# Kernel optimization log

Hardware: AMD Instinct MI355X
Metric: run time of the kernel (lower is better)

The kernel has to match this reference:

```python
import jax, jax.numpy as jnp
import numpy as np

N = 100000      # nodes per type
E = 1600000     # edges per edge type
D = 128         # input feature dim
C = 128         # hidden channels (heads=1, concat)
DE = 16         # edge feature dim
OUT = 64        # out channels
L = 2           # num conv layers
T = 2           # num edge types: 0 = user->item, 1 = item->user


def setup_inputs() -> dict:
    key = jax.random.key(0)
    ks = jax.random.split(key, 17)
    s = 0.05  # keep attention logits / activations well-scaled
    return {
        "x_user": jax.random.normal(ks[0], (N, D), jnp.float32),
        "x_item": jax.random.normal(ks[1], (N, D), jnp.float32),
        "ea_ui": jax.random.normal(ks[2], (E, DE), jnp.float32),
        "ea_iu": jax.random.normal(ks[3], (E, DE), jnp.float32),
        "W_src": jax.random.normal(ks[4], (L, T, C, C), jnp.float32) * s,
        "W_dst": jax.random.normal(ks[5], (L, T, C, C), jnp.float32) * s,
        "W_edge": jax.random.normal(ks[6], (L, T, DE, C), jnp.float32) * s,
        "att_src": jax.random.normal(ks[7], (L, T, C), jnp.float32) * s,
        "att_dst": jax.random.normal(ks[8], (L, T, C), jnp.float32) * s,
        "att_edge": jax.random.normal(ks[9], (L, T, C), jnp.float32) * s,
        "conv_bias": jax.random.normal(ks[10], (L, T, C), jnp.float32) * s,
        "lin0_W": jax.random.normal(ks[11], (2, C, C), jnp.float32) * s,
        "lin0_b": jax.random.normal(ks[12], (2, C), jnp.float32) * s,
        "lin1_W": jax.random.normal(ks[13], (2, C, OUT), jnp.float32) * s,
        "lin1_b": jax.random.normal(ks[14], (2, OUT), jnp.float32) * s,
        "ei_ui": jax.random.randint(ks[15], (2, E), 0, N, jnp.int32),
        "ei_iu": jax.random.randint(ks[16], (2, E), 0, N, jnp.int32),
    }


def _gat_conv(x_src, x_dst, ei, ea, Ws, Wd, We, a_s, a_d, a_e, b):
    """PyG GATConv((-1,-1), C, heads=1, edge_dim=DE, add_self_loops=False)."""
    row, col = ei[0], ei[1]
    hs = x_src @ Ws                      # [Ns, C]
    hd = x_dst @ Wd                      # [Nd, C]
    he = ea @ We                         # [E, C]
    a = hs @ a_s                         # [Ns] alpha_src per source node
    adst = hd @ a_d                      # [Nd] alpha_dst per dest node
    ae = he @ a_e                        # [E]
    alpha = jax.nn.leaky_relu(a[row] + adst[col] + ae, 0.2)  # [E]
    n_dst = x_dst.shape[0]
    m = jax.ops.segment_max(alpha, col, num_segments=n_dst)  # stable softmax max
    ex = jnp.exp(alpha - m[col])
    den = jax.ops.segment_sum(ex, col, num_segments=n_dst)
    w = ex / den[col]                    # edge-softmax over incoming edges
    out = jax.ops.segment_sum(w[:, None] * hs[row], col, num_segments=n_dst)
    return out + b                       # [Nd, C]


def reference(x_user, x_item, ea_ui, ea_iu, W_src, W_dst, W_edge, att_src,
              att_dst, att_edge, conv_bias, lin0_W, lin0_b, lin1_W, lin1_b,
              ei_ui, ei_iu):
    xu, xi = x_user, x_item
    for l in range(L):
        # edge type 0: user -> item ; edge type 1: item -> user
        new_item = _gat_conv(xu, xi, ei_ui, ea_ui, W_src[l, 0], W_dst[l, 0],
                             W_edge[l, 0], att_src[l, 0], att_dst[l, 0],
                             att_edge[l, 0], conv_bias[l, 0])
        new_user = _gat_conv(xi, xu, ei_iu, ea_iu, W_src[l, 1], W_dst[l, 1],
                             W_edge[l, 1], att_src[l, 1], att_dst[l, 1],
                             att_edge[l, 1], conv_bias[l, 1])
        # HeteroConv aggr='sum' has one contribution per dst type; then relu
        xu = jax.nn.relu(new_user)
        xi = jax.nn.relu(new_item)
    # HeteroDictLinear stack (no activation between, per gnn.Sequential spec)
    xu = (xu @ lin0_W[0] + lin0_b[0]) @ lin1_W[0] + lin1_b[0]
    xi = (xi @ lin0_W[1] + lin0_b[1]) @ lin1_W[1] + lin1_b[1]
    return xu, xi
```

## Files before the change

### kernel.cpp

```cpp
#include <hip/hip_runtime.h>
#include <hip/hip_fp16.h>


typedef _Float16 half4 __attribute__((ext_vector_type(4)));
typedef float f32x4 __attribute__((ext_vector_type(4)));

#define KCAP 48

__device__ __forceinline__ float wave_sum(float v){
#pragma unroll
  for (int off = 32; off; off >>= 1) v += __shfl_xor(v, off);
  return v;
}

__global__ __launch_bounds__(64) void precompute_vec_kernel(
    const float* __restrict__ Wsrc, const float* __restrict__ Wdst,
    const float* __restrict__ Wedge, const float* __restrict__ As,
    const float* __restrict__ Ad, const float* __restrict__ Ae,
    float* __restrict__ pv_as, float* __restrict__ pv_ad, float* __restrict__ pv_ae)
{
  int b = blockIdx.x;
  int lt = b / 272, rem = b - lt * 272;
  int lane = threadIdx.x;
  const float* W; const float* a; float* out;
  if (rem < 128)      { W = Wsrc  + lt*16384 + rem*128;       a = As + lt*128; out = pv_as + lt*128 + rem; }
  else if (rem < 256) { int d = rem-128; W = Wdst + lt*16384 + d*128; a = Ad + lt*128; out = pv_ad + lt*128 + d; }
  else                { int j = rem-256; W = Wedge + lt*2048 + j*128; a = Ae + lt*128; out = pv_ae + lt*16 + j; }
  float s = W[lane]*a[lane] + W[lane+64]*a[lane+64];
  s = wave_sum(s);
  if (lane == 0) *out = s;
}

__global__ void combine_linear_kernel(const float* __restrict__ lin0W, const float* __restrict__ lin0b,
                                      const float* __restrict__ lin1W, const float* __restrict__ lin1b,
                                      float* __restrict__ Wc, float* __restrict__ bc)
{
  int idx = blockIdx.x * 256 + threadIdx.x;
  if (idx < 2*128*64) {
    int t = idx / 8192; int r = (idx / 64) & 127; int o = idx & 63;
    const float* w0 = lin0W + t*16384 + r*128;
    const float* w1 = lin1W + t*8192 + o;
    float s = 0.f;
    for (int m = 0; m < 128; ++m) s += w0[m] * w1[m*64];
    Wc[idx] = s;
  } else if (idx < 2*128*64 + 128) {
    int q = idx - 16384; int t = q >> 6; int o = q & 63;
    const float* b0 = lin0b + t*128;
    const float* w1 = lin1W + t*8192 + o;
    float s = lin1b[t*64 + o];
    for (int m = 0; m < 128; ++m) s += b0[m] * w1[m*64];
    bc[q] = s;
  }
}

__global__ __launch_bounds__(256) void wfrag_prep_kernel(
    const float* __restrict__ Wsrc, const float* __restrict__ pv_as,
    const float* __restrict__ pv_ad, const float* __restrict__ Wc,
    _Float16* __restrict__ Wf_conv, _Float16* __restrict__ Wf_mlp)
{
  int idx = blockIdx.x * 256 + threadIdx.x;
  if (idx < 73728) {
    int within = idx & 255;
    int l = within >> 2, i = within & 3;
    int rest = idx >> 8;
    int c = rest % 9; int rest2 = rest / 9;
    int s = rest2 & 7; int g = rest2 >> 3;
    int lg = g >> 1, who = g & 1;
    int k = s*16 + ((l>>4)<<2) + i;
    float val = 0.f;
    if (c < 8) {
      int col = c*16 + (l & 15);
      int lt = lg*2 + who;
      val = Wsrc[(size_t)lt*16384 + k*128 + col];
    } else {
      int cc = l & 15;
      if (cc == 0)      val = pv_as[(lg*2 + who)*128 + k];
      else if (cc == 1) val = pv_ad[(lg*2 + (who^1))*128 + k];
    }
    Wf_conv[idx] = (_Float16)val;
  } else {
    int q = idx - 73728;
    int within = q & 255;
    int l = within >> 2, i = within & 3;
    int rest = q >> 8;
    int c = rest & 3; int s = (rest >> 2) & 7; int m = rest >> 5;
    int k = s*16 + ((l>>4)<<2) + i;
    int col = c*16 + (l & 15);
    Wf_mlp[q] = (_Float16)Wc[m*8192 + k*64 + col];
  }
}

__global__ __launch_bounds__(256) void bucket_fill_kernel(
    const int* __restrict__ ei0, const int* __restrict__ ei1,
    const float* __restrict__ ea0, const float* __restrict__ ea1,
    const float* __restrict__ pv_ae,
    int* __restrict__ cnt0, int* __restrict__ cnt1,
    float* __restrict__ bkt0, float* __restrict__ bkt1, int E, int gE)
{
  int b = blockIdx.x;
  int type = (b >= gE) ? 1 : 0;
  const int* ei = type ? ei1 : ei0;
  const float* ea = type ? ea1 : ea0;
  int* cnt = type ? cnt1 : cnt0;
  float* bkt = type ? bkt1 : bkt0;
  int e = (b - (type ? gE : 0)) * 256 + threadIdx.x;
  if (e >= E) return;
  int src = ei[e], col = ei[E + e];
  const float4* er = (const float4*)(ea + (size_t)e * 16);
  float4 a0 = er[0], a1 = er[1], a2 = er[2], a3 = er[3];
  const float* v0 = pv_ae + type * 16;
  const float* v1 = pv_ae + (2 + type) * 16;
  float ae0 = a0.x*v0[0] + a0.y*v0[1] + a0.z*v0[2] + a0.w*v0[3]
            + a1.x*v0[4] + a1.y*v0[5] + a1.z*v0[6] + a1.w*v0[7]
            + a2.x*v0[8] + a2.y*v0[9] + a2.z*v0[10] + a2.w*v0[11]
            + a3.x*v0[12] + a3.y*v0[13] + a3.z*v0[14] + a3.w*v0[15];
  float ae1 = a0.x*v1[0] + a0.y*v1[1] + a0.z*v1[2] + a0.w*v1[3]
            + a1.x*v1[4] + a1.y*v1[5] + a1.z*v1[6] + a1.w*v1[7]
            + a2.x*v1[8] + a2.y*v1[9] + a2.z*v1[10] + a2.w*v1[11]
            + a3.x*v1[12] + a3.y*v1[13] + a3.z*v1[14] + a3.w*v1[15];
  int pos = atomicAdd(&cnt[col], 1);
  if (pos < KCAP) {
    size_t base = ((size_t)col * KCAP + pos) * 3;
    bkt[base]     = __int_as_float(src);
    bkt[base + 1] = ae0;
    bkt[base + 2] = ae1;
  }
}

template<bool FIN, bool CONV>
__global__ __launch_bounds__(256) void gemm_mfma(
    const void* __restrict__ Xv, const uint2* __restrict__ Wf,
    void* __restrict__ Hout, float* __restrict__ asrc, float* __restrict__ adst,
    const float* __restrict__ bias, int N)
{
  constexpr int NT = CONV ? 9 : 4;
  __shared__ __align__(16) _Float16 ldsb[64 * 136];
  const int t = threadIdx.x;
  const int r0 = blockIdx.x * 64;

  if (FIN) {
    const float* X = (const float*)Xv;
    for (int v = t; v < 2048; v += 256) {
      int row = v >> 5, q = v & 31;
      int r = r0 + row;
      float4 xv = make_float4(0.f, 0.f, 0.f, 0.f);
      if (r < N) xv = *(const float4*)(X + (size_t)r * 128 + q * 4);
      _Float16* d = &ldsb[row * 136 + q * 4];
      d[0] = (_Float16)xv.x; d[1] = (_Float16)xv.y;
      d[2] = (_Float16)xv.z; d[3] = (_Float16)xv.w;
    }
  } else {
    const _Float16* X = (const _Float16*)Xv;
    for (int v = t; v < 1024; v += 256) {
      int row = v >> 4, q = v & 15;
      int r = r0 + row;
      uint4 xv = make_uint4(0u, 0u, 0u, 0u);
      if (r < N) xv = *(const uint4*)(X + (size_t)r * 128 + q * 8);
      *(uint4*)(&ldsb[row * 136 + q * 8]) = xv;
    }
  }
  __syncthreads();

  const int w = t >> 6, l = t & 63;
  f32x4 acc[NT];
#pragma unroll
  for (int c = 0; c < NT; ++c) acc[c] = (f32x4)(0.f);

  const uint2* wp = Wf + l;
  const int aoff = (w * 16 + (l & 15)) * 136 + ((l >> 4) << 2);
#pragma unroll
  for (int s = 0; s < 8; ++s) {
    half4 af = *(const half4*)(&ldsb[aoff + s * 16]);
#pragma unroll
    for (int c = 0; c < NT; ++c) {
      uint2 bw = wp[(s * NT + c) * 64];
      half4 bf = *reinterpret_cast<const half4*>(&bw);
      acc[c] = __builtin_amdgcn_mfma_f32_16x16x16f16(af, bf, acc[c], 0, 0, 0);
    }
  }
  __syncthreads();

  if (CONV) {
#pragma unroll
    for (int c = 0; c < 8; ++c)
#pragma unroll
      for (int rg = 0; rg < 4; ++rg)
        ldsb[(w*16 + ((l>>4)<<2) + rg) * 136 + c*16 + (l & 15)] = (_Float16)acc[c][rg];
    if ((l & 15) < 2) {
      float* dst = ((l & 15) == 0) ? asrc : adst;
#pragma unroll
      for (int rg = 0; rg < 4; ++rg) {
        int r = r0 + w*16 + ((l>>4)<<2) + rg;
        if (r < N) dst[r] = acc[8][rg];
      }
    }
    __syncthreads();
    _Float16* H = (_Float16*)Hout;
    for (int v = t; v < 1024; v += 256) {
      int row = v >> 4, q = v & 15;
      int r = r0 + row;
      if (r < N)
        *(uint4*)(H + (size_t)r * 128 + q * 8) = *(const uint4*)(&ldsb[row * 136 + q * 8]);
    }
  } else {
    float* ldsf = (float*)ldsb;
#pragma unroll
    for (int c = 0; c < 4; ++c)
#pragma unroll
      for (int rg = 0; rg < 4; ++rg)
        ldsf[(w*16 + ((l>>4)<<2) + rg) * 68 + c*16 + (l & 15)] = acc[c][rg];
    __syncthreads();
    float* O = (float*)Hout;
    for (int v = t; v < 1024; v += 256) {
      int row = v >> 4, q = v & 15;
      int r = r0 + row;
      if (r < N) {
        float4 o = *(const float4*)(&ldsf[row * 68 + q * 4]);
        float4 bb = *(const float4*)(bias + q * 4);
        o.x += bb.x; o.y += bb.y; o.z += bb.z; o.w += bb.w;
        *(float4*)(O + (size_t)r * 64 + q * 4) = o;
      }
    }
  }
}

__global__ __launch_bounds__(256) void aggregate_bucket(
    const int* __restrict__ cnt_tab, const float* __restrict__ bkt,
    const float* __restrict__ asrc_tab, const float* __restrict__ adst_tab,
    const __half2* __restrict__ hs, const float* __restrict__ bias,
    __half2* __restrict__ xnew, int N, int lsel)
{
  int wid = threadIdx.x >> 6, lane = threadIdx.x & 63;
  int n = blockIdx.x * 4 + wid;
  if (n >= N) return;
  int cnt = cnt_tab[n]; if (cnt > KCAP) cnt = KCAP;
  float adst = adst_tab[n];
  int r = 0; float wgt = 0.f;
  if (lane < cnt) {
    size_t base = ((size_t)n * KCAP + lane) * 3;
    r = __float_as_int(bkt[base]);
    float ae = bkt[base + 1 + lsel];
    float a = asrc_tab[r];
    float al = a + adst + ae;
    al = (al > 0.f) ? al : 0.2f * al;
    wgt = __expf(al);
  }
  float den = wave_sum(wgt);
  float acc0 = 0.f, acc1 = 0.f;
  int k = 0;
  for (; k + 8 <= cnt; k += 8) {
    int rr[8]; float ww[8]; float2 f[8];
#pragma unroll
    for (int j = 0; j < 8; ++j) { rr[j] = __shfl(r, k + j); ww[j] = __shfl(wgt, k + j); }
#pragma unroll
    for (int j = 0; j < 8; ++j) f[j] = __half22float2(hs[(size_t)rr[j] * 64 + lane]);
#pragma unroll
    for (int j = 0; j < 8; ++j) { acc0 = fmaf(ww[j], f[j].x, acc0); acc1 = fmaf(ww[j], f[j].y, acc1); }
  }
  for (; k < cnt; ++k) {
    int rr = __shfl(r, k); float ww = __shfl(wgt, k);
    float2 f = __half22float2(hs[(size_t)rr * 64 + lane]);
    acc0 = fmaf(ww, f.x, acc0); acc1 = fmaf(ww, f.y, acc1);
  }
  float b0 = bias[2*lane], b1 = bias[2*lane + 1];
  float o0 = b0, o1 = b1;
  if (den > 0.f) {
    float inv = 1.f / den;
    o0 = fmaf(acc0, inv, b0);
    o1 = fmaf(acc1, inv, b1);
  }
  o0 = fmaxf(o0, 0.f);
  o1 = fmaxf(o1, 0.f);
  xnew[(size_t)n * 64 + lane] = __floats2half2_rn(o0, o1);
}

extern "C" void kernel_launch(void* const* d_in, const int* in_sizes, int n_in,
                              void* d_out, int out_size, void* d_ws, size_t ws_size,
                              hipStream_t stream)
{
  const float* x_user   = (const float*)d_in[0];
  const float* x_item   = (const float*)d_in[1];
  const float* ea_ui    = (const float*)d_in[2];
  const float* ea_iu    = (const float*)d_in[3];
  const float* W_src    = (const float*)d_in[4];
  const float* W_dst    = (const float*)d_in[5];
  const float* W_edge   = (const float*)d_in[6];
  const float* att_src  = (const float*)d_in[7];
  const float* att_dst  = (const float*)d_in[8];
  const float* att_edge = (const float*)d_in[9];
  const float* conv_bias= (const float*)d_in[10];
  const float* lin0W    = (const float*)d_in[11];
  const float* lin0b    = (const float*)d_in[12];
  const float* lin1W    = (const float*)d_in[13];
  const float* lin1b    = (const float*)d_in[14];
  const int*   ei_ui    = (const int*)d_in[15];
  const int*   ei_iu    = (const int*)d_in[16];

  const int N = in_sizes[0] / 128;
  const int E = in_sizes[15] / 2;

  char* p = (char*)d_ws;
  auto alloc = [&](size_t bytes) -> void* {
    void* r = (void*)p;
    p += (bytes + 255) & ~(size_t)255;
    return r;
  };
  _Float16* xu_a = (_Float16*)alloc((size_t)N * 128 * 2);
  _Float16* xi_a = (_Float16*)alloc((size_t)N * 128 * 2);
  _Float16* xi_b = (_Float16*)alloc((size_t)N * 128 * 2);
  _Float16* hs_u = (_Float16*)alloc((size_t)N * 128 * 2);
  _Float16* hs_i = (_Float16*)alloc((size_t)N * 128 * 2);
  float* bkt_ui  = (float*)alloc((size_t)N * KCAP * 12);
  float* bkt_iu  = (float*)alloc((size_t)N * KCAP * 12);
  int*   cnt_ui  = (int*)alloc((size_t)2 * N * 4);
  int*   cnt_iu  = cnt_ui + N;
  float* asrc_u  = (float*)alloc((size_t)N * 4);
  float* adst_u  = (float*)alloc((size_t)N * 4);
  float* asrc_i  = (float*)alloc((size_t)N * 4);
  float* adst_i  = (float*)alloc((size_t)N * 4);
  float* pv_as   = (float*)alloc(512 * 4);
  float* pv_ad   = (float*)alloc(512 * 4);
  float* pv_ae   = (float*)alloc(64 * 4);
  float* Wc      = (float*)alloc(2 * 128 * 64 * 4);
  float* bc      = (float*)alloc(128 * 4);
  _Float16* Wf_conv = (_Float16*)alloc(73728 * 2);
  _Float16* Wf_mlp  = (_Float16*)alloc(16384 * 2);
  _Float16* xu_b = hs_u;

  precompute_vec_kernel<<<4 * 272, 64, 0, stream>>>(W_src, W_dst, W_edge,
      att_src, att_dst, att_edge, pv_as, pv_ad, pv_ae);
  combine_linear_kernel<<<65, 256, 0, stream>>>(lin0W, lin0b, lin1W, lin1b, Wc, bc);
  wfrag_prep_kernel<<<352, 256, 0, stream>>>(W_src, pv_as, pv_ad, Wc, Wf_conv, Wf_mlp);

  const int gE = (E + 255) / 256;
  hipMemsetAsync(cnt_ui, 0, (size_t)2 * N * 4, stream);
  bucket_fill_kernel<<<2 * gE, 256, 0, stream>>>(ei_ui, ei_iu, ea_ui, ea_iu,
      pv_ae, cnt_ui, cnt_iu, bkt_ui, bkt_iu, E, gE);

  const int gB  = (N + 63) / 64;
  const int gN4 = (N + 3) / 4;
  const uint2* Wfc = (const uint2*)Wf_conv;
  const uint2* Wfm = (const uint2*)Wf_mlp;

  gemm_mfma<true, true><<<gB, 256, 0, stream>>>(x_user, Wfc + 0*4608, hs_u, asrc_u, adst_u, nullptr, N);
  gemm_mfma<true, true><<<gB, 256, 0, stream>>>(x_item, Wfc + 1*4608, hs_i, asrc_i, adst_i, nullptr, N);
  aggregate_bucket<<<gN4, 256, 0, stream>>>(cnt_ui, bkt_ui, asrc_u, adst_i,
      (const __half2*)hs_u, conv_bias + 0*128, (__half2*)xi_a, N, 0);
  aggregate_bucket<<<gN4, 256, 0, stream>>>(cnt_iu, bkt_iu, asrc_i, adst_u,
      (const __half2*)hs_i, conv_bias + 1*128, (__half2*)xu_a, N, 0);

  gemm_mfma<false, true><<<gB, 256, 0, stream>>>(xu_a, Wfc + 2*4608, hs_u, asrc_u, adst_u, nullptr, N);
  gemm_mfma<false, true><<<gB, 256, 0, stream>>>(xi_a, Wfc + 3*4608, hs_i, asrc_i, adst_i, nullptr, N);
  aggregate_bucket<<<gN4, 256, 0, stream>>>(cnt_ui, bkt_ui, asrc_u, adst_i,
      (const __half2*)hs_u, conv_bias + 2*128, (__half2*)xi_b, N, 1);
  aggregate_bucket<<<gN4, 256, 0, stream>>>(cnt_iu, bkt_iu, asrc_i, adst_u,
      (const __half2*)hs_i, conv_bias + 3*128, (__half2*)xu_b, N, 1);

  float* out = (float*)d_out;
  gemm_mfma<false, false><<<gB, 256, 0, stream>>>(xu_b, Wfm + 0,    out,                  nullptr, nullptr, bc,      N);
  gemm_mfma<false, false><<<gB, 256, 0, stream>>>(xi_b, Wfm + 2048, out + (size_t)N * 64, nullptr, nullptr, bc + 64, N);
}
```

Measured before the change: 596.3 us.

## Merge per-type launches and overlap first GEMM with bucket fill; pack buckets

Folds the layer-0 input GEMMs and the edge bucket fill into a single interleaved launch, so the compute-bound GEMM blocks run alongside the atomic-heavy fill blocks. Paired user/item GEMMs and aggregations each become one launch. Bucket entries shrink from three floats to one uint2 (src index plus two fp16 edge logits), which cuts fill-write and aggregate-read traffic. Risks are fp16 rounding of the edge attention terms and a mixed-role kernel whose LDS footprint is also paid by fill blocks.

```diff
diff --git a/kernel.cpp b/kernel.cpp
--- a/kernel.cpp
+++ b/kernel.cpp
@@ -90,20 +90,20 @@
   }
 }
 
-__global__ __launch_bounds__(256) void bucket_fill_kernel(
+__device__ __forceinline__ void fill_body(
+    int fid, int tid,
     const int* __restrict__ ei0, const int* __restrict__ ei1,
     const float* __restrict__ ea0, const float* __restrict__ ea1,
     const float* __restrict__ pv_ae,
     int* __restrict__ cnt0, int* __restrict__ cnt1,
-    float* __restrict__ bkt0, float* __restrict__ bkt1, int E, int gE)
-{
-  int b = blockIdx.x;
-  int type = (b >= gE) ? 1 : 0;
+    uint2* __restrict__ bkt0, uint2* __restrict__ bkt1, int E, int gEf)
+{
+  int type = (fid >= gEf) ? 1 : 0;
   const int* ei = type ? ei1 : ei0;
   const float* ea = type ? ea1 : ea0;
   int* cnt = type ? cnt1 : cnt0;
-  float* bkt = type ? bkt1 : bkt0;
-  int e = (b - (type ? gE : 0)) * 256 + threadIdx.x;
+  uint2* bkt = type ? bkt1 : bkt0;
+  int e = (fid - type * gEf) * 256 + tid;
   if (e >= E) return;
   int src = ei[e], col = ei[E + e];
   const float4* er = (const float4*)(ea + (size_t)e * 16);
@@ -120,23 +120,22 @@
             + a3.x*v1[12] + a3.y*v1[13] + a3.z*v1[14] + a3.w*v1[15];
   int pos = atomicAdd(&cnt[col], 1);
   if (pos < KCAP) {
-    size_t base = ((size_t)col * KCAP + pos) * 3;
-    bkt[base]     = __int_as_float(src);
-    bkt[base + 1] = ae0;
-    bkt[base + 2] = ae1;
+    __half2 hh = __floats2half2_rn(ae0, ae1);
+    uint2 val;
+    val.x = (unsigned)src;
+    val.y = *(const unsigned*)&hh;
+    bkt[(size_t)col * KCAP + pos] = val;
   }
 }
 
 template<bool FIN, bool CONV>
-__global__ __launch_bounds__(256) void gemm_mfma(
+__device__ __forceinline__ void gemm_body(_Float16* ldsb, int blk, int t,
     const void* __restrict__ Xv, const uint2* __restrict__ Wf,
     void* __restrict__ Hout, float* __restrict__ asrc, float* __restrict__ adst,
     const float* __restrict__ bias, int N)
 {
   constexpr int NT = CONV ? 9 : 4;
-  __shared__ __align__(16) _Float16 ldsb[64 * 136];
-  const int t = threadIdx.x;
-  const int r0 = blockIdx.x * 64;
+  const int r0 = blk * 64;
 
   if (FIN) {
     const float* X = (const float*)Xv;
@@ -224,22 +223,84 @@
   }
 }
 
-__global__ __launch_bounds__(256) void aggregate_bucket(
-    const int* __restrict__ cnt_tab, const float* __restrict__ bkt,
-    const float* __restrict__ asrc_tab, const float* __restrict__ adst_tab,
-    const __half2* __restrict__ hs, const float* __restrict__ bias,
-    __half2* __restrict__ xnew, int N, int lsel)
-{
+__global__ __launch_bounds__(256) void phase0_kernel(
+    const float* __restrict__ xu, const float* __restrict__ xi,
+    const uint2* __restrict__ Wfc,
+    _Float16* __restrict__ hs_u, _Float16* __restrict__ hs_i,
+    float* __restrict__ asrc_u, float* __restrict__ adst_u,
+    float* __restrict__ asrc_i, float* __restrict__ adst_i,
+    const int* __restrict__ ei0, const int* __restrict__ ei1,
+    const float* __restrict__ ea0, const float* __restrict__ ea1,
+    const float* __restrict__ pv_ae,
+    int* __restrict__ cnt0, int* __restrict__ cnt1,
+    uint2* __restrict__ bkt0, uint2* __restrict__ bkt1,
+    int N, int E, int gB, int P, int gEf)
+{
+  __shared__ __align__(16) _Float16 ldsb[64 * 136];
+  int b = blockIdx.x, t = threadIdx.x;
+  int g = b / P, r = b - g * P;
+  if (r == 0) {
+    if (g < gB)
+      gemm_body<true, true>(ldsb, g, t, xu, Wfc, hs_u, asrc_u, adst_u, nullptr, N);
+    else
+      gemm_body<true, true>(ldsb, g - gB, t, xi, Wfc + 4608, hs_i, asrc_i, adst_i, nullptr, N);
+  } else {
+    int fid = b - g - 1;
+    if (fid < 2 * gEf)
+      fill_body(fid, t, ei0, ei1, ea0, ea1, pv_ae, cnt0, cnt1, bkt0, bkt1, E, gEf);
+  }
+}
+
+template<bool FIN, bool CONV>
+__global__ __launch_bounds__(256) void gemm_pair_kernel(
+    const void* __restrict__ X0, const void* __restrict__ X1,
+    const uint2* __restrict__ Wf0, const uint2* __restrict__ Wf1,
+    void* __restrict__ H0, void* __restrict__ H1,
+    float* __restrict__ asrc0, float* __restrict__ adst0,
+    float* __restrict__ asrc1, float* __restrict__ adst1,
+    const float* __restrict__ bias0, const float* __restrict__ bias1,
+    int N, int gB)
+{
+  __shared__ __align__(16) _Float16 ldsb[64 * 136];
+  int b = blockIdx.x;
+  if (b < gB)
+    gemm_body<FIN, CONV>(ldsb, b, threadIdx.x, X0, Wf0, H0, asrc0, adst0, bias0, N);
+  else
+    gemm_body<FIN, CONV>(ldsb, b - gB, threadIdx.x, X1, Wf1, H1, asrc1, adst1, bias1, N);
+}
+
+__global__ __launch_bounds__(256) void aggregate_pair(
+    const int* __restrict__ cnt0, const uint2* __restrict__ bkt0,
+    const float* __restrict__ asrc0, const float* __restrict__ adst0,
+    const __half2* __restrict__ hs0, const float* __restrict__ bias0,
+    __half2* __restrict__ out0,
+    const int* __restrict__ cnt1, const uint2* __restrict__ bkt1,
+    const float* __restrict__ asrc1, const float* __restrict__ adst1,
+    const __half2* __restrict__ hs1, const float* __restrict__ bias1,
+    __half2* __restrict__ out1,
+    int N, int lsel, int gHalf)
+{
+  int b = blockIdx.x;
+  int tt = (b >= gHalf) ? 1 : 0;
+  const int* cnt_tab = tt ? cnt1 : cnt0;
+  const uint2* bkt   = tt ? bkt1 : bkt0;
+  const float* asrc_tab = tt ? asrc1 : asrc0;
+  const float* adst_tab = tt ? adst1 : adst0;
+  const __half2* hs  = tt ? hs1 : hs0;
+  const float* bias  = tt ? bias1 : bias0;
+  __half2* xnew      = tt ? out1 : out0;
+
   int wid = threadIdx.x >> 6, lane = threadIdx.x & 63;
-  int n = blockIdx.x * 4 + wid;
+  int n = (b - tt * gHalf) * 4 + wid;
   if (n >= N) return;
   int cnt = cnt_tab[n]; if (cnt > KCAP) cnt = KCAP;
   float adst = adst_tab[n];
   int r = 0; float wgt = 0.f;
   if (lane < cnt) {
-    size_t base = ((size_t)n * KCAP + lane) * 3;
-    r = __float_as_int(bkt[base]);
-    float ae = bkt[base + 1 + lsel];
+    uint2 sv = bkt[(size_t)n * KCAP + lane];
+    r = (int)sv.x;
+    __half2 hh = *(const __half2*)&sv.y;
+    float ae = lsel ? __high2float(hh) : __low2float(hh);
     float a = asrc_tab[r];
     float al = a + adst + ae;
     al = (al > 0.f) ? al : 0.2f * al;
@@ -307,11 +368,12 @@
   };
   _Float16* xu_a = (_Float16*)alloc((size_t)N * 128 * 2);
   _Float16* xi_a = (_Float16*)alloc((size_t)N * 128 * 2);
+  _Float16* xu_b = (_Float16*)alloc((size_t)N * 128 * 2);
   _Float16* xi_b = (_Float16*)alloc((size_t)N * 128 * 2);
   _Float16* hs_u = (_Float16*)alloc((size_t)N * 128 * 2);
   _Float16* hs_i = (_Float16*)alloc((size_t)N * 128 * 2);
-  float* bkt_ui  = (float*)alloc((size_t)N * KCAP * 12);
-  float* bkt_iu  = (float*)alloc((size_t)N * KCAP * 12);
+  uint2* bkt_ui  = (uint2*)alloc((size_t)N * KCAP * 8);
+  uint2* bkt_iu  = (uint2*)alloc((size_t)N * KCAP * 8);
   int*   cnt_ui  = (int*)alloc((size_t)2 * N * 4);
   int*   cnt_iu  = cnt_ui + N;
   float* asrc_u  = (float*)alloc((size_t)N * 4);
@@ -325,38 +387,42 @@
   float* bc      = (float*)alloc(128 * 4);
   _Float16* Wf_conv = (_Float16*)alloc(73728 * 2);
   _Float16* Wf_mlp  = (_Float16*)alloc(16384 * 2);
-  _Float16* xu_b = hs_u;
 
   precompute_vec_kernel<<<4 * 272, 64, 0, stream>>>(W_src, W_dst, W_edge,
       att_src, att_dst, att_edge, pv_as, pv_ad, pv_ae);
   combine_linear_kernel<<<65, 256, 0, stream>>>(lin0W, lin0b, lin1W, lin1b, Wc, bc);
   wfrag_prep_kernel<<<352, 256, 0, stream>>>(W_src, pv_as, pv_ad, Wc, Wf_conv, Wf_mlp);
-
-  const int gE = (E + 255) / 256;
   hipMemsetAsync(cnt_ui, 0, (size_t)2 * N * 4, stream);
-  bucket_fill_kernel<<<2 * gE, 256, 0, stream>>>(ei_ui, ei_iu, ea_ui, ea_iu,
-      pv_ae, cnt_ui, cnt_iu, bkt_ui, bkt_iu, E, gE);
-
+
+  const int gEf = (E + 255) / 256;
   const int gB  = (N + 63) / 64;
+  const int GB2 = 2 * gB;
+  const int P   = 1 + (2 * gEf + GB2 - 1) / GB2;
   const int gN4 = (N + 3) / 4;
   const uint2* Wfc = (const uint2*)Wf_conv;
   const uint2* Wfm = (const uint2*)Wf_mlp;
 
-  gemm_mfma<true, true><<<gB, 256, 0, stream>>>(x_user, Wfc + 0*4608, hs_u, asrc_u, adst_u, nullptr, N);
-  gemm_mfma<true, true><<<gB, 256, 0, stream>>>(x_item, Wfc + 1*4608, hs_i, asrc_i, adst_i, nullptr, N);
-  aggregate_bucket<<<gN4, 256, 0, stream>>>(cnt_ui, bkt_ui, asrc_u, adst_i,
-      (const __half2*)hs_u, conv_bias + 0*128, (__half2*)xi_a, N, 0);
-  aggregate_bucket<<<gN4, 256, 0, stream>>>(cnt_iu, bkt_iu, asrc_i, adst_u,
-      (const __half2*)hs_i, conv_bias + 1*128, (__half2*)xu_a, N, 0);
-
-  gemm_mfma<false, true><<<gB, 256, 0, stream>>>(xu_a, Wfc + 2*4608, hs_u, asrc_u, adst_u, nullptr, N);
-  gemm_mfma<false, true><<<gB, 256, 0, stream>>>(xi_a, Wfc + 3*4608, hs_i, asrc_i, adst_i, nullptr, N);
-  aggregate_bucket<<<gN4, 256, 0, stream>>>(cnt_ui, bkt_ui, asrc_u, adst_i,
-      (const __half2*)hs_u, conv_bias + 2*128, (__half2*)xi_b, N, 1);
-  aggregate_bucket<<<gN4, 256, 0, stream>>>(cnt_iu, bkt_iu, asrc_i, adst_u,
-      (const __half2*)hs_i, conv_bias + 3*128, (__half2*)xu_b, N, 1);
+  phase0_kernel<<<P * GB2, 256, 0, stream>>>(x_user, x_item, Wfc,
+      hs_u, hs_i, asrc_u, adst_u, asrc_i, adst_i,
+      ei_ui, ei_iu, ea_ui, ea_iu, pv_ae, cnt_ui, cnt_iu, bkt_ui, bkt_iu,
+      N, E, gB, P, gEf);
+
+  aggregate_pair<<<2 * gN4, 256, 0, stream>>>(
+      cnt_ui, bkt_ui, asrc_u, adst_i, (const __half2*)hs_u, conv_bias + 0*128, (__half2*)xi_a,
+      cnt_iu, bkt_iu, asrc_i, adst_u, (const __half2*)hs_i, conv_bias + 1*128, (__half2*)xu_a,
+      N, 0, gN4);
+
+  gemm_pair_kernel<false, true><<<GB2, 256, 0, stream>>>(
+      xu_a, xi_a, Wfc + 2*4608, Wfc + 3*4608, hs_u, hs_i,
+      asrc_u, adst_u, asrc_i, adst_i, nullptr, nullptr, N, gB);
+
+  aggregate_pair<<<2 * gN4, 256, 0, stream>>>(
+      cnt_ui, bkt_ui, asrc_u, adst_i, (const __half2*)hs_u, conv_bias + 2*128, (__half2*)xi_b,
+      cnt_iu, bkt_iu, asrc_i, adst_u, (const __half2*)hs_i, conv_bias + 3*128, (__half2*)xu_b,
+      N, 1, gN4);
 
   float* out = (float*)d_out;
-  gemm_mfma<false, false><<<gB, 256, 0, stream>>>(xu_b, Wfm + 0,    out,                  nullptr, nullptr, bc,      N);
-  gemm_mfma<false, false><<<gB, 256, 0, stream>>>(xi_b, Wfm + 2048, out + (size_t)N * 64, nullptr, nullptr, bc + 64, N);
-}
+  gemm_pair_kernel<false, false><<<GB2, 256, 0, stream>>>(
+      xu_b, xi_b, Wfm, Wfm + 2048, out, out + (size_t)N * 64,
+      nullptr, nullptr, nullptr, nullptr, bc, bc + 64, N, gB);
+}
```

New measurement: 516.5 us. 1.15x faster.
